# Kernel tuning notes

Hardware: AMD Instinct MI355X
Metric: run time of the kernel (lower is better)

The kernel has to match this reference:

```python
import jax, jax.numpy as jnp
import numpy as np

# DenseKAN defaults from tfkan
GRID_SIZE = 5
SPLINE_ORDER = 3
GRID_MIN, GRID_MAX = -1.0, 1.0
KH = KW = 3  # kernel_size


def _grid():
    h = (GRID_MAX - GRID_MIN) / GRID_SIZE
    # grid_size + 2*spline_order + 1 knots, extended beyond grid_range
    return jnp.linspace(GRID_MIN - SPLINE_ORDER * h, GRID_MAX + SPLINE_ORDER * h,
                        GRID_SIZE + 2 * SPLINE_ORDER + 1, dtype=jnp.float32)


def _spline_basis(x, grid, order):
    # x: (N, in_size) -> (N, in_size, grid_size + spline_order) via Cox-de Boor
    x = x[..., None]
    b = ((x >= grid[:-1]) & (x < grid[1:])).astype(x.dtype)
    for k in range(1, order + 1):
        b = ((x - grid[:-(k + 1)]) / (grid[k:-1] - grid[:-(k + 1)]) * b[..., :-1]
             + (grid[k + 1:] - x) / (grid[k + 1:] - grid[1:-k]) * b[..., 1:])
    return b


def _extract_patches(x):
    # VALID, stride 1; TF extract_patches flattens feature dim as [kh, kw, C]
    B, H, W, C = x.shape
    Ho, Wo = H - KH + 1, W - KW + 1
    p = jnp.stack([x[:, di:di + Ho, dj:dj + Wo, :]
                   for di in range(KH) for dj in range(KW)], axis=3)  # (B,Ho,Wo,KH*KW,C)
    return p.reshape(B, Ho, Wo, KH * KW * C)


def setup_inputs() -> dict:
    key = jax.random.key(0)
    k = jax.random.split(key, 5)
    B, H, W, C = 32, 32, 32, 32
    F = 128
    in_size = KH * KW * C
    basis = GRID_SIZE + SPLINE_ORDER
    return {
        "x": jax.random.normal(k[0], (B, H, W, C), jnp.float32),
        "spline_kernel": jax.random.normal(k[1], (in_size, basis, F), jnp.float32) * 0.1,
        "scale_factor": jax.random.normal(k[2], (in_size, F), jnp.float32) * 0.1,
        "kan_bias": jnp.zeros((F,), jnp.float32),
        "conv_bias": jnp.zeros((F,), jnp.float32),
    }


def reference(x, spline_kernel, scale_factor, kan_bias, conv_bias):
    grid = _grid()
    pat = _extract_patches(x)                 # (B, Ho, Wo, in_size)
    B, Ho, Wo, In = pat.shape
    xf = pat.reshape(-1, In)                  # (N, in_size)
    sb = _spline_basis(xf, grid, SPLINE_ORDER)  # (N, in_size, basis)
    # phi(x) = scale * (spline(x) + silu(x)); output = sum_i phi_i + biases
    # fused: never materialize the (N, in_size, units) tensor
    w = spline_kernel * scale_factor[:, None, :]        # (in_size, basis, units)
    out = (jnp.einsum('nik,iko->no', sb, w)
           + jax.nn.silu(xf) @ scale_factor
           + kan_bias)                                   # (N, units)
    out = out.reshape(B, Ho, Wo, -1) + conv_bias
    return out
```

## Files before the change

### kernel.cpp

```cpp
#include <hip/hip_runtime.h>
#include <hip/hip_bf16.h>


#define C_IN   32
#define F_OUT  128
#define BATCH  32
#define HIN    32
#define WIN    32
#define HO_    30
#define WO_    30
#define NPIX   (BATCH*HO_*WO_)
#define NELEM  (BATCH*HIN*WIN*C_IN)
#define NBASIS 9
#define KCHUNKS 81
#define FEAT_BYTES  ((size_t)NELEM*NBASIS*2)
#define WPACK_BYTES ((size_t)KCHUNKS*F_OUT*32*2)

typedef __attribute__((ext_vector_type(8))) short short8;
typedef __attribute__((ext_vector_type(4))) float f32x4;

__device__ __forceinline__ short bf16_bits(float v) {
  return __builtin_bit_cast(short, __float2bfloat16(v));
}

#define GLOAD_LDS16(g, l) \
  __builtin_amdgcn_global_load_lds((const __attribute__((address_space(1))) void*)(g), \
                                   (__attribute__((address_space(3))) void*)(l), 16, 0, 0)

__device__ __forceinline__ void kan_basis(float v, float* o9) {
  float b0[11], b1[10], b2[9];
#pragma unroll
  for (int j = 0; j < 11; ++j) {
    float gj  = -2.2f + 0.4f * (float)j;
    float gj1 = -2.2f + 0.4f * (float)(j + 1);
    b0[j] = (v >= gj && v < gj1) ? 1.0f : 0.0f;
  }
#pragma unroll
  for (int j = 0; j < 10; ++j) {
    float gj = -2.2f + 0.4f * (float)j;
    b1[j] = (v - gj) * 2.5f * b0[j] + ((gj + 0.8f) - v) * 2.5f * b0[j + 1];
  }
#pragma unroll
  for (int j = 0; j < 9; ++j) {
    float gj = -2.2f + 0.4f * (float)j;
    b2[j] = (v - gj) * 1.25f * b1[j] + ((gj + 1.2f) - v) * 1.25f * b1[j + 1];
  }
#pragma unroll
  for (int j = 0; j < 8; ++j) {
    float gj = -2.2f + 0.4f * (float)j;
    o9[j] = (v - gj) * (1.0f/1.2f) * b2[j] + ((gj + 1.6f) - v) * (1.0f/1.2f) * b2[j + 1];
  }
  o9[8] = v / (1.0f + __expf(-v));
}

__global__ __launch_bounds__(256) void kan_featurize(
    const float* __restrict__ x, __hip_bfloat16* __restrict__ feat) {
  int t = blockIdx.x * 256 + threadIdx.x;
  int bhw = t >> 2, c0 = (t & 3) * 8;
  const f32x4* xp = (const f32x4*)(x + ((size_t)bhw * 32 + c0));
  f32x4 v0 = xp[0], v1 = xp[1];
  float f[8][9];
#pragma unroll
  for (int j = 0; j < 4; ++j) kan_basis(v0[j], f[j]);
#pragma unroll
  for (int j = 0; j < 4; ++j) kan_basis(v1[j], f[4 + j]);

  char* o = (char*)feat + (size_t)bhw * 576 + c0 * 2;
#pragma unroll
  for (int k = 0; k < 9; ++k) {
    short8 s;
#pragma unroll
    for (int j = 0; j < 8; ++j)
      s[j] = bf16_bits(f[j][k]);
    *(short8*)(o + k * 64) = s;
  }
}

__global__ __launch_bounds__(256) void kan_pack_w(
    const float* __restrict__ sk, const float* __restrict__ sf,
    __hip_bfloat16* __restrict__ wp) {
  int t = blockIdx.x * 256 + threadIdx.x;
  int part = t & 3;
  int col  = (t >> 2) & 127;
  int kc   = t >> 9;
  int dd = kc / 9, k = kc - dd * 9;
  short8 s;
#pragma unroll
  for (int j = 0; j < 8; ++j) {
    int i = dd * 32 + part * 8 + j;
    float w = sf[i * 128 + col];
    if (k < 8) w *= sk[(i * 8 + k) * 128 + col];
    s[j] = bf16_bits(w);
  }
  int slot = part ^ ((col >> 1) & 3);
  *(short8*)((char*)wp + (size_t)kc * 8192 + col * 64 + slot * 16) = s;
}

__global__ __launch_bounds__(256) void kan_gemm(
    const __hip_bfloat16* __restrict__ featb, const __hip_bfloat16* __restrict__ wpb,
    const float* __restrict__ kbias, const float* __restrict__ cbias,
    float* __restrict__ out) {
  __shared__ char lds[73728];
  const char* feat = (const char*)featb;
  const char* wp   = (const char*)wpb;

  int tid  = threadIdx.x;
  int lane = tid & 63, wid = tid >> 6;
  int wm = wid >> 1, wn = wid & 1;
  int q = lane >> 4, fr = lane & 15;

  int orig = blockIdx.x;
  int xcd = orig & 7, sub = orig >> 3;
  int swz = (xcd < 2 ? xcd * 57 : 114 + (xcd - 2) * 56) + sub;
  int mb = swz * 64;

  int arow = tid >> 2, aslot = tid & 3;
  int apix = mb + arow;
  int wo = apix % 30, t30 = apix / 30;
  int ho = t30 % 30,  bb  = t30 / 30;
  const char* asrc = feat + (size_t)((bb * 32 + ho) * 32 + wo) * 576
                          + (size_t)((aslot ^ ((arow >> 1) & 3)) * 16);

  int ar0 = 32 * wm + fr, ar1 = ar0 + 16;
  int aoff0 = ar0 * 64 + ((q ^ ((ar0 >> 1) & 3)) * 16);
  int aoff1 = ar1 * 64 + ((q ^ ((ar1 >> 1) & 3)) * 16);
  int boff[4];
#pragma unroll
  for (int n = 0; n < 4; ++n) {
    int col = 64 * wn + 16 * n + fr;
    boff[n] = col * 64 + ((q ^ ((col >> 1) & 3)) * 16);
  }

  f32x4 acc[2][4];
#pragma unroll
  for (int m = 0; m < 2; ++m)
#pragma unroll
    for (int n = 0; n < 4; ++n) acc[m][n] = (f32x4)(0.0f);

  auto stage = [&](int kc) {
    int s = kc % 6;
    int dd = kc / 9, k = kc - dd * 9;
    int di = dd / 3, dj = dd - di * 3;
    int au = (di * 32 + dj) * 576 + k * 64;
    GLOAD_LDS16(asrc + au, lds + s * 4096 + tid * 16);
    const char* wsrc = wp + (size_t)kc * 8192 + tid * 16;
    GLOAD_LDS16(wsrc,        lds + 24576 + s * 8192 + tid * 16);
    GLOAD_LDS16(wsrc + 4096, lds + 24576 + s * 8192 + 4096 + tid * 16);
  };

  auto compute = [&](int s) {
    const char* A = lds + s * 4096;
    const char* B = lds + 24576 + s * 8192;
    short8 a0 = *(const short8*)(A + aoff0);
    short8 a1 = *(const short8*)(A + aoff1);
    __builtin_amdgcn_s_setprio(1);
#pragma unroll
    for (int n = 0; n < 4; ++n) {
      short8 bn = *(const short8*)(B + boff[n]);
      acc[0][n] = __builtin_amdgcn_mfma_f32_16x16x32_bf16(a0, bn, acc[0][n], 0, 0, 0);
      acc[1][n] = __builtin_amdgcn_mfma_f32_16x16x32_bf16(a1, bn, acc[1][n], 0, 0, 0);
    }
    __builtin_amdgcn_s_setprio(0);
  };

  stage(0); stage(1); stage(2); stage(3); stage(4);
  asm volatile("s_waitcnt vmcnt(12)" ::: "memory");
  __builtin_amdgcn_s_barrier();
  __builtin_amdgcn_sched_barrier(0);

  for (int kc = 0; kc < KCHUNKS - 5; ++kc) {
    stage(kc + 5);
    compute(kc % 6);
    asm volatile("s_waitcnt vmcnt(12) lgkmcnt(0)" ::: "memory");
    __builtin_amdgcn_s_barrier();
    __builtin_amdgcn_sched_barrier(0);
  }
  asm volatile("s_waitcnt vmcnt(0)" ::: "memory");
  __builtin_amdgcn_s_barrier();
  __builtin_amdgcn_sched_barrier(0);
  compute((KCHUNKS - 5) % 6);
  compute((KCHUNKS - 4) % 6);
  compute((KCHUNKS - 3) % 6);
  compute((KCHUNKS - 2) % 6);
  compute((KCHUNKS - 1) % 6);

#pragma unroll
  for (int n = 0; n < 4; ++n) {
    int col = 64 * wn + 16 * n + fr;
    float bias = kbias[col] + cbias[col];
#pragma unroll
    for (int m = 0; m < 2; ++m) {
      int row = mb + 32 * wm + 16 * m + q * 4;
      f32x4 v = acc[m][n];
#pragma unroll
      for (int r = 0; r < 4; ++r)
        out[(size_t)(row + r) * 128 + col] = v[r] + bias;
    }
  }
}

extern "C" void kernel_launch(void* const* d_in, const int* in_sizes, int n_in,
                              void* d_out, int out_size, void* d_ws, size_t ws_size,
                              hipStream_t stream) {
  const float* x  = (const float*)d_in[0];
  const float* sk = (const float*)d_in[1];
  const float* sf = (const float*)d_in[2];
  const float* kb = (const float*)d_in[3];
  const float* cb = (const float*)d_in[4];
  float* out = (float*)d_out;

  char* ws = (char*)d_ws;
  __hip_bfloat16* feat = (__hip_bfloat16*)ws;
  __hip_bfloat16* wpk  = (__hip_bfloat16*)(ws + FEAT_BYTES);

  hipLaunchKernelGGL(kan_featurize, dim3(NELEM / 8 / 256), dim3(256), 0, stream, x, feat);
  hipLaunchKernelGGL(kan_pack_w, dim3((KCHUNKS * F_OUT * 32 / 8) / 256), dim3(256), 0, stream,
                     sk, sf, wpk);
  hipLaunchKernelGGL(kan_gemm, dim3(NPIX / 64), dim3(256), 0, stream,
                     feat, wpk, kb, cb, out);
}
```

Measured before the change: 114.6 us.

## Process two K-chunks per barrier with triple-buffered super-stages

```diff
diff --git a/kernel.cpp b/kernel.cpp
--- a/kernel.cpp
+++ b/kernel.cpp
@@ -12,7 +12,8 @@
 #define NPIX   (BATCH*HO_*WO_)
 #define NELEM  (BATCH*HIN*WIN*C_IN)
 #define NBASIS 9
-#define KCHUNKS 81
+#define KCHUNKS 82
+#define NSUPER 41
 #define FEAT_BYTES  ((size_t)NELEM*NBASIS*2)
 #define WPACK_BYTES ((size_t)KCHUNKS*F_OUT*32*2)
 
@@ -87,9 +88,12 @@
   short8 s;
 #pragma unroll
   for (int j = 0; j < 8; ++j) {
-    int i = dd * 32 + part * 8 + j;
-    float w = sf[i * 128 + col];
-    if (k < 8) w *= sk[(i * 8 + k) * 128 + col];
+    float w = 0.0f;
+    if (kc < 81) {
+      int i = dd * 32 + part * 8 + j;
+      w = sf[i * 128 + col];
+      if (k < 8) w *= sk[(i * 8 + k) * 128 + col];
+    }
     s[j] = bf16_bits(w);
   }
   int slot = part ^ ((col >> 1) & 3);
@@ -137,52 +141,58 @@
 #pragma unroll
     for (int n = 0; n < 4; ++n) acc[m][n] = (f32x4)(0.0f);
 
-  auto stage = [&](int kc) {
-    int s = kc % 6;
-    int dd = kc / 9, k = kc - dd * 9;
-    int di = dd / 3, dj = dd - di * 3;
-    int au = (di * 32 + dj) * 576 + k * 64;
-    GLOAD_LDS16(asrc + au, lds + s * 4096 + tid * 16);
-    const char* wsrc = wp + (size_t)kc * 8192 + tid * 16;
-    GLOAD_LDS16(wsrc,        lds + 24576 + s * 8192 + tid * 16);
-    GLOAD_LDS16(wsrc + 4096, lds + 24576 + s * 8192 + 4096 + tid * 16);
+  auto stage = [&](int t) {
+    int s = t % 3;
+#pragma unroll
+    for (int h = 0; h < 2; ++h) {
+      int kc = 2 * t + h;
+      int kcl = kc < 81 ? kc : 80;
+      int dd = kcl / 9, k = kcl - dd * 9;
+      int di = dd / 3, dj = dd - di * 3;
+      int au = (di * 32 + dj) * 576 + k * 64;
+      GLOAD_LDS16(asrc + au, lds + s * 8192 + h * 4096 + tid * 16);
+      const char* wsrc = wp + (size_t)kc * 8192 + tid * 16;
+      GLOAD_LDS16(wsrc,        lds + 24576 + s * 16384 + h * 8192 + tid * 16);
+      GLOAD_LDS16(wsrc + 4096, lds + 24576 + s * 16384 + h * 8192 + 4096 + tid * 16);
+    }
   };
 
-  auto compute = [&](int s) {
-    const char* A = lds + s * 4096;
-    const char* B = lds + 24576 + s * 8192;
-    short8 a0 = *(const short8*)(A + aoff0);
-    short8 a1 = *(const short8*)(A + aoff1);
+  auto compute = [&](int t) {
+    int s = t % 3;
     __builtin_amdgcn_s_setprio(1);
 #pragma unroll
-    for (int n = 0; n < 4; ++n) {
-      short8 bn = *(const short8*)(B + boff[n]);
-      acc[0][n] = __builtin_amdgcn_mfma_f32_16x16x32_bf16(a0, bn, acc[0][n], 0, 0, 0);
-      acc[1][n] = __builtin_amdgcn_mfma_f32_16x16x32_bf16(a1, bn, acc[1][n], 0, 0, 0);
+    for (int h = 0; h < 2; ++h) {
+      const char* A = lds + s * 8192 + h * 4096;
+      const char* B = lds + 24576 + s * 16384 + h * 8192;
+      short8 a0 = *(const short8*)(A + aoff0);
+      short8 a1 = *(const short8*)(A + aoff1);
+#pragma unroll
+      for (int n = 0; n < 4; ++n) {
+        short8 bn = *(const short8*)(B + boff[n]);
+        acc[0][n] = __builtin_amdgcn_mfma_f32_16x16x32_bf16(a0, bn, acc[0][n], 0, 0, 0);
+        acc[1][n] = __builtin_amdgcn_mfma_f32_16x16x32_bf16(a1, bn, acc[1][n], 0, 0, 0);
+      }
     }
     __builtin_amdgcn_s_setprio(0);
   };
 
-  stage(0); stage(1); stage(2); stage(3); stage(4);
-  asm volatile("s_waitcnt vmcnt(12)" ::: "memory");
+  stage(0); stage(1);
+  asm volatile("s_waitcnt vmcnt(6)" ::: "memory");
   __builtin_amdgcn_s_barrier();
   __builtin_amdgcn_sched_barrier(0);
 
-  for (int kc = 0; kc < KCHUNKS - 5; ++kc) {
-    stage(kc + 5);
-    compute(kc % 6);
-    asm volatile("s_waitcnt vmcnt(12) lgkmcnt(0)" ::: "memory");
+  for (int t = 0; t < NSUPER - 2; ++t) {
+    stage(t + 2);
+    compute(t);
+    asm volatile("s_waitcnt vmcnt(6) lgkmcnt(0)" ::: "memory");
     __builtin_amdgcn_s_barrier();
     __builtin_amdgcn_sched_barrier(0);
   }
   asm volatile("s_waitcnt vmcnt(0)" ::: "memory");
   __builtin_amdgcn_s_barrier();
   __builtin_amdgcn_sched_barrier(0);
-  compute((KCHUNKS - 5) % 6);
-  compute((KCHUNKS - 4) % 6);
-  compute((KCHUNKS - 3) % 6);
-  compute((KCHUNKS - 2) % 6);
-  compute((KCHUNKS - 1) % 6);
+  compute(NSUPER - 2);
+  compute(NSUPER - 1);
 
 #pragma unroll
   for (int n = 0; n < 4; ++n) {
```

New measurement: 114.6 us. Within noise of the previous version (+0.0%).

## Merge prep kernels and restructure GEMM to 2-wave blocks with register-held B

Applied to the files above, without the earlier changes.

```diff
diff --git a/kernel.cpp b/kernel.cpp
--- a/kernel.cpp
+++ b/kernel.cpp
@@ -5,16 +5,12 @@
 #define C_IN   32
 #define F_OUT  128
 #define BATCH  32
-#define HIN    32
-#define WIN    32
-#define HO_    30
-#define WO_    30
-#define NPIX   (BATCH*HO_*WO_)
-#define NELEM  (BATCH*HIN*WIN*C_IN)
-#define NBASIS 9
-#define KCHUNKS 81
-#define FEAT_BYTES  ((size_t)NELEM*NBASIS*2)
-#define WPACK_BYTES ((size_t)KCHUNKS*F_OUT*32*2)
+#define NPIX   28800
+#define NELEM  1048576
+#define KREAL  81
+#define KALLOC 84
+#define FEAT_BYTES  ((size_t)NELEM*9*2)
+#define WPACK_BYTES ((size_t)KALLOC*F_OUT*32*2)
 
 typedef __attribute__((ext_vector_type(8))) short short8;
 typedef __attribute__((ext_vector_type(4))) float f32x4;
@@ -53,60 +49,60 @@
   o9[8] = v / (1.0f + __expf(-v));
 }
 
-__global__ __launch_bounds__(256) void kan_featurize(
-    const float* __restrict__ x, __hip_bfloat16* __restrict__ feat) {
-  int t = blockIdx.x * 256 + threadIdx.x;
-  int bhw = t >> 2, c0 = (t & 3) * 8;
-  const f32x4* xp = (const f32x4*)(x + ((size_t)bhw * 32 + c0));
-  f32x4 v0 = xp[0], v1 = xp[1];
-  float f[8][9];
-#pragma unroll
-  for (int j = 0; j < 4; ++j) kan_basis(v0[j], f[j]);
-#pragma unroll
-  for (int j = 0; j < 4; ++j) kan_basis(v1[j], f[4 + j]);
-
-  char* o = (char*)feat + (size_t)bhw * 576 + c0 * 2;
-#pragma unroll
-  for (int k = 0; k < 9; ++k) {
+__global__ __launch_bounds__(256) void kan_producer(
+    const float* __restrict__ x, const float* __restrict__ sk,
+    const float* __restrict__ sf, __hip_bfloat16* __restrict__ feat,
+    __hip_bfloat16* __restrict__ wp) {
+  if (blockIdx.x < 512) {
+    int t = blockIdx.x * 256 + threadIdx.x;
+    int bhw = t >> 2, c0 = (t & 3) * 8;
+    const f32x4* xp = (const f32x4*)(x + ((size_t)bhw * 32 + c0));
+    f32x4 v0 = xp[0], v1 = xp[1];
+    float f[8][9];
+#pragma unroll
+    for (int j = 0; j < 4; ++j) kan_basis(v0[j], f[j]);
+#pragma unroll
+    for (int j = 0; j < 4; ++j) kan_basis(v1[j], f[4 + j]);
+    char* o = (char*)feat + (size_t)bhw * 576 + c0 * 2;
+#pragma unroll
+    for (int k = 0; k < 9; ++k) {
+      short8 s;
+#pragma unroll
+      for (int j = 0; j < 8; ++j) s[j] = bf16_bits(f[j][k]);
+      *(short8*)(o + k * 64) = s;
+    }
+  } else {
+    int t = (blockIdx.x - 512) * 256 + threadIdx.x;
+    int part = t & 3;
+    int col  = (t >> 2) & 127;
+    int kc   = t >> 9;
+    int dd = kc / 9, k = kc - dd * 9;
     short8 s;
 #pragma unroll
-    for (int j = 0; j < 8; ++j)
-      s[j] = bf16_bits(f[j][k]);
-    *(short8*)(o + k * 64) = s;
-  }
-}
-
-__global__ __launch_bounds__(256) void kan_pack_w(
-    const float* __restrict__ sk, const float* __restrict__ sf,
-    __hip_bfloat16* __restrict__ wp) {
-  int t = blockIdx.x * 256 + threadIdx.x;
-  int part = t & 3;
-  int col  = (t >> 2) & 127;
-  int kc   = t >> 9;
-  int dd = kc / 9, k = kc - dd * 9;
-  short8 s;
-#pragma unroll
-  for (int j = 0; j < 8; ++j) {
-    int i = dd * 32 + part * 8 + j;
-    float w = sf[i * 128 + col];
-    if (k < 8) w *= sk[(i * 8 + k) * 128 + col];
-    s[j] = bf16_bits(w);
-  }
-  int slot = part ^ ((col >> 1) & 3);
-  *(short8*)((char*)wp + (size_t)kc * 8192 + col * 64 + slot * 16) = s;
-}
-
-__global__ __launch_bounds__(256) void kan_gemm(
+    for (int j = 0; j < 8; ++j) {
+      float w = 0.0f;
+      if (kc < KREAL) {
+        int i = dd * 32 + part * 8 + j;
+        w = sf[i * 128 + col];
+        if (k < 8) w *= sk[(i * 8 + k) * 128 + col];
+      }
+      s[j] = bf16_bits(w);
+    }
+    int slot = part ^ ((col >> 1) & 3);
+    *(short8*)((char*)wp + (size_t)kc * 8192 + col * 64 + slot * 16) = s;
+  }
+}
+
+__global__ __launch_bounds__(128) void kan_gemm(
     const __hip_bfloat16* __restrict__ featb, const __hip_bfloat16* __restrict__ wpb,
     const float* __restrict__ kbias, const float* __restrict__ cbias,
     float* __restrict__ out) {
-  __shared__ char lds[73728];
+  __shared__ char lds[12288];
   const char* feat = (const char*)featb;
   const char* wp   = (const char*)wpb;
 
   int tid  = threadIdx.x;
-  int lane = tid & 63, wid = tid >> 6;
-  int wm = wid >> 1, wn = wid & 1;
+  int lane = tid & 63, wn = tid >> 6;
   int q = lane >> 4, fr = lane & 15;
 
   int orig = blockIdx.x;
@@ -114,89 +110,95 @@
   int swz = (xcd < 2 ? xcd * 57 : 114 + (xcd - 2) * 56) + sub;
   int mb = swz * 64;
 
-  int arow = tid >> 2, aslot = tid & 3;
-  int apix = mb + arow;
-  int wo = apix % 30, t30 = apix / 30;
-  int ho = t30 % 30,  bb  = t30 / 30;
-  const char* asrc = feat + (size_t)((bb * 32 + ho) * 32 + wo) * 576
-                          + (size_t)((aslot ^ ((arow >> 1) & 3)) * 16);
-
-  int ar0 = 32 * wm + fr, ar1 = ar0 + 16;
-  int aoff0 = ar0 * 64 + ((q ^ ((ar0 >> 1) & 3)) * 16);
-  int aoff1 = ar1 * 64 + ((q ^ ((ar1 >> 1) & 3)) * 16);
-  int boff[4];
-#pragma unroll
-  for (int n = 0; n < 4; ++n) {
-    int col = 64 * wn + 16 * n + fr;
-    boff[n] = col * 64 + ((q ^ ((col >> 1) & 3)) * 16);
-  }
-
-  f32x4 acc[2][4];
-#pragma unroll
-  for (int m = 0; m < 2; ++m)
+  int r0 = tid >> 2;
+  int p  = (tid & 3) ^ ((r0 >> 1) & 3);
+  int pixa = mb + r0, pixb = mb + 32 + r0;
+  int woa = pixa % 30, ta = pixa / 30, hoa = ta % 30, ba = ta / 30;
+  int wob = pixb % 30, tb_ = pixb / 30, hob = tb_ % 30, bb = tb_ / 30;
+  const char* asrc0 = feat + (size_t)((ba * 32 + hoa) * 32 + woa) * 576 + p * 16;
+  const char* asrc1 = feat + (size_t)((bb * 32 + hob) * 32 + wob) * 576 + p * 16;
+
+  int aoff[4];
+#pragma unroll
+  for (int m = 0; m < 4; ++m) {
+    int row = 16 * m + fr;
+    aoff[m] = row * 64 + ((q ^ ((row >> 1) & 3)) * 16);
+  }
+
+  const char* bptr = wp + (size_t)(64 * wn + fr) * 64 + ((q ^ ((fr >> 1) & 3)) * 16);
+
+  f32x4 acc[4][4];
+#pragma unroll
+  for (int m = 0; m < 4; ++m)
 #pragma unroll
     for (int n = 0; n < 4; ++n) acc[m][n] = (f32x4)(0.0f);
 
-  auto stage = [&](int kc) {
-    int s = kc % 6;
-    int dd = kc / 9, k = kc - dd * 9;
-    int di = dd / 3, dj = dd - di * 3;
-    int au = (di * 32 + dj) * 576 + k * 64;
-    GLOAD_LDS16(asrc + au, lds + s * 4096 + tid * 16);
-    const char* wsrc = wp + (size_t)kc * 8192 + tid * 16;
-    GLOAD_LDS16(wsrc,        lds + 24576 + s * 8192 + tid * 16);
-    GLOAD_LDS16(wsrc + 4096, lds + 24576 + s * 8192 + 4096 + tid * 16);
-  };
-
-  auto compute = [&](int s) {
-    const char* A = lds + s * 4096;
-    const char* B = lds + 24576 + s * 8192;
-    short8 a0 = *(const short8*)(A + aoff0);
-    short8 a1 = *(const short8*)(A + aoff1);
-    __builtin_amdgcn_s_setprio(1);
-#pragma unroll
-    for (int n = 0; n < 4; ++n) {
-      short8 bn = *(const short8*)(B + boff[n]);
-      acc[0][n] = __builtin_amdgcn_mfma_f32_16x16x32_bf16(a0, bn, acc[0][n], 0, 0, 0);
-      acc[1][n] = __builtin_amdgcn_mfma_f32_16x16x32_bf16(a1, bn, acc[1][n], 0, 0, 0);
-    }
-    __builtin_amdgcn_s_setprio(0);
-  };
-
-  stage(0); stage(1); stage(2); stage(3); stage(4);
-  asm volatile("s_waitcnt vmcnt(12)" ::: "memory");
+  short8 br[3][4];
+
+#define STAGEA(KC, S) do {                                                   \
+    int kc_ = (KC) > 80 ? 80 : (KC);                                         \
+    int dd_ = kc_ / 9, kk_ = kc_ - dd_ * 9;                                  \
+    int di_ = dd_ / 3, dj_ = dd_ - di_ * 3;                                  \
+    int au_ = (di_ * 32 + dj_) * 576 + kk_ * 64;                             \
+    GLOAD_LDS16(asrc0 + au_, lds + (S) * 4096 + tid * 16);                   \
+    GLOAD_LDS16(asrc1 + au_, lds + (S) * 4096 + 2048 + tid * 16);            \
+  } while (0)
+
+#define LOADB(KC, S) do {                                                    \
+    _Pragma("unroll")                                                        \
+    for (int n = 0; n < 4; ++n)                                              \
+      br[S][n] = *(const short8*)(bptr + (size_t)(KC) * 8192 + n * 1024);    \
+  } while (0)
+
+#define GBODY(T, S0, S1, S2) do {                                            \
+    LOADB((T) + 2, S2);                                                      \
+    STAGEA((T) + 2, S2);                                                     \
+    __builtin_amdgcn_s_setprio(1);                                           \
+    _Pragma("unroll")                                                        \
+    for (int m = 0; m < 4; ++m) {                                            \
+      short8 am = *(const short8*)(lds + (S0) * 4096 + aoff[m]);             \
+      _Pragma("unroll")                                                      \
+      for (int n = 0; n < 4; ++n)                                            \
+        acc[m][n] = __builtin_amdgcn_mfma_f32_16x16x32_bf16(                 \
+            am, br[S0][n], acc[m][n], 0, 0, 0);                              \
+    }                                                                        \
+    __builtin_amdgcn_s_setprio(0);                                           \
+    asm volatile("s_waitcnt vmcnt(6) lgkmcnt(0)" ::: "memory");              \
+    __builtin_amdgcn_s_barrier();                                            \
+    __builtin_amdgcn_sched_barrier(0);                                       \
+  } while (0)
+
+  STAGEA(0, 0);
+  STAGEA(1, 1);
+  LOADB(0, 0);
+  LOADB(1, 1);
+  asm volatile("s_waitcnt vmcnt(4)" ::: "memory");
   __builtin_amdgcn_s_barrier();
   __builtin_amdgcn_sched_barrier(0);
 
-  for (int kc = 0; kc < KCHUNKS - 5; ++kc) {
-    stage(kc + 5);
-    compute(kc % 6);
-    asm volatile("s_waitcnt vmcnt(12) lgkmcnt(0)" ::: "memory");
-    __builtin_amdgcn_s_barrier();
-    __builtin_amdgcn_sched_barrier(0);
-  }
-  asm volatile("s_waitcnt vmcnt(0)" ::: "memory");
-  __builtin_amdgcn_s_barrier();
-  __builtin_amdgcn_sched_barrier(0);
-  compute((KCHUNKS - 5) % 6);
-  compute((KCHUNKS - 4) % 6);
-  compute((KCHUNKS - 3) % 6);
-  compute((KCHUNKS - 2) % 6);
-  compute((KCHUNKS - 1) % 6);
+  for (int tb = 0; tb < 27; ++tb) {
+    int t0 = 3 * tb;
+    GBODY(t0,     0, 1, 2);
+    GBODY(t0 + 1, 1, 2, 0);
+    GBODY(t0 + 2, 2, 0, 1);
+  }
 
 #pragma unroll
   for (int n = 0; n < 4; ++n) {
     int col = 64 * wn + 16 * n + fr;
     float bias = kbias[col] + cbias[col];
 #pragma unroll
-    for (int m = 0; m < 2; ++m) {
-      int row = mb + 32 * wm + 16 * m + q * 4;
+    for (int m = 0; m < 4; ++m) {
+      int row = mb + 16 * m + q * 4;
       f32x4 v = acc[m][n];
 #pragma unroll
       for (int r = 0; r < 4; ++r)
         out[(size_t)(row + r) * 128 + col] = v[r] + bias;
     }
   }
+#undef GBODY
+#undef LOADB
+#undef STAGEA
 }
 
 extern "C" void kernel_launch(void* const* d_in, const int* in_sizes, int n_in,
@@ -213,9 +215,8 @@
   __hip_bfloat16* feat = (__hip_bfloat16*)ws;
   __hip_bfloat16* wpk  = (__hip_bfloat16*)(ws + FEAT_BYTES);
 
-  hipLaunchKernelGGL(kan_featurize, dim3(NELEM / 8 / 256), dim3(256), 0, stream, x, feat);
-  hipLaunchKernelGGL(kan_pack_w, dim3((KCHUNKS * F_OUT * 32 / 8) / 256), dim3(256), 0, stream,
-                     sk, sf, wpk);
-  hipLaunchKernelGGL(kan_gemm, dim3(NPIX / 64), dim3(256), 0, stream,
+  hipLaunchKernelGGL(kan_producer, dim3(512 + 168), dim3(256), 0, stream,
+                     x, sk, sf, feat, wpk);
+  hipLaunchKernelGGL(kan_gemm, dim3(NPIX / 64), dim3(128), 0, stream,
                      feat, wpk, kb, cb, out);
 }
```

Result: no change. 116.9 us (+2.0%).
